# Performance work log

Measured on AMD Instinct MI355X. Metric: run time of the kernel, lower is better.

## Reference

```python
import jax, jax.numpy as jnp
import numpy as np

N_NODES = 50000
N_EDGES = 800000
D_IN = 128
D_OUT = 128
N_TYPES = 4
LN_EPS = 1e-5


def setup_inputs() -> dict:
    key = jax.random.key(0)
    ks = jax.random.split(key, 12)
    s1 = 1.0 / np.sqrt(2 * D_IN)
    s2 = 1.0 / np.sqrt(D_OUT)
    return {
        "x": jax.random.normal(ks[0], (N_NODES, D_IN), jnp.float32),
        "edge_index": jax.random.randint(ks[1], (2, N_EDGES), 0, N_NODES, jnp.int32),
        "edge_attr": jax.random.randint(ks[2], (N_EDGES,), 0, N_TYPES, jnp.int32),
        # per-edge-type 2-layer MLP params, stacked over type axis
        "edge_w1": jax.random.uniform(ks[3], (N_TYPES, 2 * D_IN, D_OUT), jnp.float32, -s1, s1),
        "edge_b1": jax.random.uniform(ks[4], (N_TYPES, D_OUT), jnp.float32, -s1, s1),
        "edge_w2": jax.random.uniform(ks[5], (N_TYPES, D_OUT, D_OUT), jnp.float32, -s2, s2),
        "edge_b2": jax.random.uniform(ks[6], (N_TYPES, D_OUT), jnp.float32, -s2, s2),
        "self_w": jax.random.uniform(ks[7], (D_IN, D_OUT), jnp.float32, -s2, s2),
        "self_b": jax.random.uniform(ks[8], (D_OUT,), jnp.float32, -s2, s2),
        "ln_gamma": jnp.ones((D_OUT,), jnp.float32),
        "ln_beta": jnp.zeros((D_OUT,), jnp.float32),
    }


def reference(x, edge_index, edge_attr, edge_w1, edge_b1, edge_w2, edge_b2, self_w, self_b, ln_gamma, ln_beta):
    row, col = edge_index[0], edge_index[1]
    out = x @ self_w + self_b  # (N, D_OUT) self-loop

    # gather once: (E, 2*D_IN)
    ef = jnp.concatenate([x[row], x[col]], axis=1)

    # per-edge-type MLP; masked edges contribute exactly zero, matching the
    # boolean-mask + index_add_ semantics of the original.
    msg = jnp.zeros((ef.shape[0], edge_w2.shape[-1]), dtype=x.dtype)
    for t in range(edge_w1.shape[0]):
        h = jax.nn.relu(ef @ edge_w1[t] + edge_b1[t])
        m = h @ edge_w2[t] + edge_b2[t]
        msg = msg + jnp.where((edge_attr == t)[:, None], m, 0.0)

    out = out + jax.ops.segment_sum(msg, col, num_segments=x.shape[0])

    # ReLU then LayerNorm over feature dim
    h = jax.nn.relu(out)
    mu = jnp.mean(h, axis=-1, keepdims=True)
    var = jnp.mean(jnp.square(h - mu), axis=-1, keepdims=True)
    return (h - mu) * jax.lax.rsqrt(var + LN_EPS) * ln_gamma + ln_beta
```

## Files before the change

kernel.cpp:

```cpp
#include <hip/hip_runtime.h>

#define N_NODES 50000
#define N_EDGES 800000
#define D_IN 128
#define D_OUT 128
#define N_TYPES 4
#define LN_EPS 1e-5f
#define N_BUCKETS (N_TYPES * N_NODES)
#define NJT 9

#define NBIN 196
#define BIN_CAP 8192
#define TILE_A 2048
#define NBA ((N_EDGES + TILE_A - 1) / TILE_A)

typedef __attribute__((ext_vector_type(4))) float f32x4;
typedef __attribute__((ext_vector_type(8))) __bf16 bf16x8;
typedef __attribute__((ext_vector_type(8))) unsigned short u16x8;

constexpr size_t wsal(size_t x) { return (x + 255) & ~size_t(255); }
constexpr size_t OFF_PTR    = 0;
constexpr size_t OFF_BCUR   = OFF_PTR   + wsal((size_t)(N_BUCKETS + 1) * 4);
constexpr size_t OFF_BINBUF = OFF_BCUR  + wsal((size_t)256 * 4);
constexpr size_t OFF_SROWS  = OFF_BINBUF + wsal((size_t)NBIN * BIN_CAP * 4);
constexpr size_t OFF_XB     = OFF_SROWS + wsal((size_t)N_EDGES * 4);
constexpr size_t OFF_WCAT   = OFF_XB    + wsal((size_t)N_NODES * D_IN * 2);
constexpr size_t OFF_BIAS   = OFF_WCAT  + wsal((size_t)NJT * 4 * 128 * 32 * 2);
constexpr size_t OFF_W2T    = OFF_BIAS  + wsal((size_t)NJT * 128 * 4);
constexpr size_t OFF_XAB    = OFF_W2T   + wsal((size_t)N_TYPES * 4 * 128 * 32 * 2);
constexpr size_t OFF_S      = OFF_XAB   + wsal((size_t)8 * N_NODES * 128 * 2);
constexpr size_t WS_TOTAL   = OFF_S     + wsal((size_t)N_BUCKETS * 128 * 2);

__device__ __forceinline__ unsigned short f2bf(float f) {
    unsigned int u = __builtin_bit_cast(unsigned int, f);
    u += 0x7FFFu + ((u >> 16) & 1u);
    return (unsigned short)(u >> 16);
}
__device__ __forceinline__ float bf2f_lo(unsigned int u) { return __builtin_bit_cast(float, u << 16); }
__device__ __forceinline__ float bf2f_hi(unsigned int u) { return __builtin_bit_cast(float, u & 0xFFFF0000u); }

#define PREP_N0 (NJT * 4 * 128 * 32)
#define PREP_N1 (NJT * 128)
#define PREP_N2 (N_TYPES * 4 * 128 * 32)
#define NB_CVT  (N_NODES * D_IN / 4 / 256)
#define NB_PREP ((PREP_N0 + PREP_N1 + PREP_N2 + 255) / 256)

__global__ __launch_bounds__(256) void k_prep_all(
    const float* __restrict__ x,
    const float* __restrict__ w1, const float* __restrict__ sw,
    const float* __restrict__ b1, const float* __restrict__ sb,
    const float* __restrict__ w2,
    unsigned short* __restrict__ xb,
    unsigned short* __restrict__ wcatT, float* __restrict__ bias,
    unsigned short* __restrict__ w2T)
{
    const int bx = blockIdx.x;
    const int tid = threadIdx.x;
    if (bx < NB_CVT) {
        int i = bx * 256 + tid;
        const float4 v = reinterpret_cast<const float4*>(x)[i];
        ushort4 o;
        o.x = f2bf(v.x); o.y = f2bf(v.y); o.z = f2bf(v.z); o.w = f2bf(v.w);
        reinterpret_cast<ushort4*>(xb)[i] = o;
        return;
    }
    int gid = (bx - NB_CVT) * 256 + tid;
    if (gid < PREP_N0) {
        int kk = gid & 31;
        int jm = (gid >> 5) & 127;
        int ks = (gid >> 12) & 3;
        int jt = gid >> 14;
        int k  = ks * 32 + kk;
        float v;
        if (jt < 8) {
            int t = jt >> 1, half = jt & 1;
            v = w1[((size_t)t * 256 + half * 128 + k) * 128 + jm];
        } else {
            v = sw[(size_t)k * 128 + jm];
        }
        wcatT[gid] = f2bf(v);
        return;
    }
    gid -= PREP_N0;
    if (gid < PREP_N1) {
        int jt = gid >> 7, jm = gid & 127;
        float v = 0.f;
        if (jt < 8) { if (jt & 1) v = b1[(jt >> 1) * 128 + jm]; }
        else v = sb[jm];
        bias[gid] = v;
        return;
    }
    gid -= PREP_N1;
    if (gid < PREP_N2) {
        int kk = gid & 31;
        int f  = (gid >> 5) & 127;
        int ks = (gid >> 12) & 3;
        int t  = gid >> 14;
        float v = w2[((size_t)t * 128 + ks * 32 + kk) * 128 + f];
        w2T[gid] = f2bf(v);
    }
}

__global__ __launch_bounds__(256) void k_binA(
    const int* __restrict__ ei, const int* __restrict__ attr,
    int* __restrict__ binCur, unsigned int* __restrict__ binBuf)
{
    __shared__ int hist[NBIN];
    __shared__ int base[NBIN];
    const int tid = threadIdx.x;
    const int e0 = blockIdx.x * TILE_A;
    if (tid < NBIN) hist[tid] = 0;
    __syncthreads();
    #pragma unroll
    for (int it = 0; it < TILE_A / 256; ++it) {
        int e = e0 + it * 256 + tid;
        if (e < N_EDGES) atomicAdd(&hist[ei[N_EDGES + e] >> 8], 1);
    }
    __syncthreads();
    if (tid < NBIN) {
        base[tid] = atomicAdd(&binCur[tid], hist[tid]);
        hist[tid] = 0;
    }
    __syncthreads();
    #pragma unroll
    for (int it = 0; it < TILE_A / 256; ++it) {
        int e = e0 + it * 256 + tid;
        if (e < N_EDGES) {
            int c = ei[N_EDGES + e];
            int t = attr[e];
            int row = ei[e];
            int bin = c >> 8;
            int lr = atomicAdd(&hist[bin], 1);
            int dst = base[bin] + lr;
            unsigned int rec = ((unsigned int)(c & 255) << 21) | ((unsigned int)t << 19)
                             | (unsigned int)(2 * t * N_NODES + row);
            if (dst < BIN_CAP) binBuf[(size_t)bin * BIN_CAP + dst] = rec;
        }
    }
}

__global__ __launch_bounds__(256) void k_binB(
    const unsigned int* __restrict__ binBuf, const int* __restrict__ binCur,
    int* __restrict__ ptr, int* __restrict__ srows)
{
    __shared__ unsigned int recs[BIN_CAP];
    __shared__ int stage[BIN_CAP];
    __shared__ int boff[1024];
    __shared__ int sred[256];
    const int b = blockIdx.x, tid = threadIdx.x;
    const int cntb = min(binCur[b], BIN_CAP);

    for (int i = tid; i < cntb; i += 256)
        recs[i] = binBuf[(size_t)b * BIN_CAP + i];

    int myv = (tid < NBIN && tid < b) ? binCur[tid] : 0;
    sred[tid] = myv;
    __syncthreads();
    #pragma unroll
    for (int d = 128; d > 0; d >>= 1) {
        if (tid < d) sred[tid] += sred[tid + d];
        __syncthreads();
    }
    const int binBase = sred[0];
    __syncthreads();

    for (int k = tid; k < 1024; k += 256) boff[k] = 0;
    __syncthreads();
    for (int i = tid; i < cntb; i += 256)
        atomicAdd(&boff[(recs[i] >> 19) & 1023], 1);
    __syncthreads();

    const int c0 = boff[tid * 4], c1 = boff[tid * 4 + 1], c2 = boff[tid * 4 + 2], c3 = boff[tid * 4 + 3];
    const int ts = c0 + c1 + c2 + c3;
    sred[tid] = ts;
    __syncthreads();
    #pragma unroll
    for (int d = 1; d < 256; d <<= 1) {
        int add = (tid >= d) ? sred[tid - d] : 0;
        __syncthreads();
        sred[tid] += add;
        __syncthreads();
    }
    const int run = sred[tid] - ts;
    const int o0 = run, o1 = run + c0, o2 = run + c0 + c1, o3 = run + c0 + c1 + c2;
    boff[tid * 4 + 0] = o0; boff[tid * 4 + 1] = o1;
    boff[tid * 4 + 2] = o2; boff[tid * 4 + 3] = o3;
    const int gb = b * 1024 + tid * 4;
    if (gb + 3 < N_BUCKETS) {
        int4 pv; pv.x = binBase + o0; pv.y = binBase + o1; pv.z = binBase + o2; pv.w = binBase + o3;
        *reinterpret_cast<int4*>(ptr + gb) = pv;
    } else {
        if (gb + 0 < N_BUCKETS) ptr[gb + 0] = binBase + o0;
        if (gb + 1 < N_BUCKETS) ptr[gb + 1] = binBase + o1;
        if (gb + 2 < N_BUCKETS) ptr[gb + 2] = binBase + o2;
        if (gb + 3 < N_BUCKETS) ptr[gb + 3] = binBase + o3;
    }
    if (b == 0 && tid == 0) ptr[N_BUCKETS] = N_EDGES;
    __syncthreads();

    for (int i = tid; i < cntb; i += 256) {
        unsigned int r = recs[i];
        int pos = atomicAdd(&boff[(r >> 19) & 1023], 1);
        stage[pos] = (int)(r & 0x7FFFFu);
    }
    __syncthreads();
    for (int i = tid; i < cntb; i += 256)
        srows[binBase + i] = stage[i];
}

__global__ __launch_bounds__(256, 2) void k_gemm1(
    const unsigned short* __restrict__ xb,
    const unsigned short* __restrict__ wcatT,
    const float* __restrict__ bias,
    unsigned short* __restrict__ xab)
{
    const int nb = blockIdx.x * 128;
    const int jt = blockIdx.y;

    __shared__ __align__(16) unsigned short sX[128 * 136];
    __shared__ __align__(16) unsigned short sW[4 * 128 * 32];

    const int tid = threadIdx.x;
    const int lane = tid & 63;
    const int w = tid >> 6;
    const int g = lane >> 4;
    const int c = lane & 15;
    const int wf = w >> 1;
    const int we = w & 1;

    #pragma unroll
    for (int it = 0; it < 8; ++it) {
        int row = 16 * it + (tid >> 4);
        int node = min(nb + row, N_NODES - 1);
        const u16x8 v = *reinterpret_cast<const u16x8*>(xb + (size_t)node * D_IN + (tid & 15) * 8);
        *reinterpret_cast<u16x8*>(&sX[row * 136 + (tid & 15) * 8]) = v;
    }
    {
        const u16x8* gsrc = reinterpret_cast<const u16x8*>(wcatT + (size_t)jt * 16384);
        u16x8* ldst = reinterpret_cast<u16x8*>(sW);
        #pragma unroll
        for (int it = 0; it < 8; ++it)
            ldst[tid + 256 * it] = gsrc[tid + 256 * it];
    }

    f32x4 acc[4][4];
    #pragma unroll
    for (int ft = 0; ft < 4; ++ft)
        #pragma unroll
        for (int et = 0; et < 4; ++et)
            acc[ft][et] = f32x4{0.f, 0.f, 0.f, 0.f};

    __syncthreads();

    #pragma unroll
    for (int ks = 0; ks < 4; ++ks) {
        bf16x8 af[4], bfr[4];
        #pragma unroll
        for (int ft = 0; ft < 4; ++ft)
            af[ft] = *reinterpret_cast<const bf16x8*>(&sW[ks * 4096 + (64 * wf + 16 * ft + c) * 32 + 8 * g]);
        #pragma unroll
        for (int et = 0; et < 4; ++et)
            bfr[et] = *reinterpret_cast<const bf16x8*>(&sX[(64 * we + 16 * et + c) * 136 + ks * 32 + 8 * g]);
        #pragma unroll
        for (int ft = 0; ft < 4; ++ft)
            #pragma unroll
            for (int et = 0; et < 4; ++et)
                acc[ft][et] = __builtin_amdgcn_mfma_f32_16x16x32_bf16(af[ft], bfr[et], acc[ft][et], 0, 0, 0);
    }
    __syncthreads();

    {
        float bv[4][4];
        #pragma unroll
        for (int ft = 0; ft < 4; ++ft)
            #pragma unroll
            for (int r = 0; r < 4; ++r)
                bv[ft][r] = bias[jt * 128 + 64 * wf + 16 * ft + 4 * g + r];
        unsigned int* so = reinterpret_cast<unsigned int*>(sX);
        #pragma unroll
        for (int ft = 0; ft < 4; ++ft) {
            #pragma unroll
            for (int et = 0; et < 4; ++et) {
                int n = 64 * we + 16 * et + c;
                int jb = 32 * wf + 8 * ft + 2 * g;
                float v0 = acc[ft][et][0] + bv[ft][0];
                float v1 = acc[ft][et][1] + bv[ft][1];
                float v2 = acc[ft][et][2] + bv[ft][2];
                float v3 = acc[ft][et][3] + bv[ft][3];
                so[n * 68 + jb + 0] = (unsigned int)f2bf(v0) | ((unsigned int)f2bf(v1) << 16);
                so[n * 68 + jb + 1] = (unsigned int)f2bf(v2) | ((unsigned int)f2bf(v3) << 16);
            }
        }
    }
    __syncthreads();

    #pragma unroll
    for (int it = 0; it < 8; ++it) {
        int row = 16 * it + (tid >> 4);
        int node = nb + row;
        if (node < N_NODES) {
            const u16x8 v = *reinterpret_cast<const u16x8*>(&sX[row * 136 + (tid & 15) * 8]);
            *reinterpret_cast<u16x8*>(xab + ((size_t)jt * N_NODES + node) * 128 + (tid & 15) * 8) = v;
        }
    }
}

__global__ __launch_bounds__(256) void k_agg(const unsigned short* __restrict__ xab,
                                             const int* __restrict__ ptr,
                                             const int* __restrict__ srows,
                                             unsigned short* __restrict__ S)
{
    const int n = (blockIdx.x * 256 + threadIdx.x) >> 6;
    if (n >= N_NODES) return;
    const int lane = threadIdx.x & 63;
    const unsigned int* x32 = reinterpret_cast<const unsigned int*>(xab);

    int seg[5];
    #pragma unroll
    for (int t = 0; t < 5; ++t)
        seg[t] = __builtin_amdgcn_readfirstlane(ptr[4 * n + t]);

    float xbl[4], xbh[4];
    #pragma unroll
    for (int t = 0; t < 4; ++t) {
        unsigned int v = x32[((size_t)(2 * t + 1) * N_NODES + n) * 64 + lane];
        xbl[t] = bf2f_lo(v); xbh[t] = bf2f_hi(v);
    }

    float al[4] = {0.f, 0.f, 0.f, 0.f}, ah[4] = {0.f, 0.f, 0.f, 0.f};

    #pragma unroll
    for (int t = 0; t < 4; ++t) {
        const int lo = seg[t], hi = seg[t + 1];
        int j = lo;
        for (; j + 4 <= hi; j += 4) {
            int a0 = __builtin_amdgcn_readfirstlane(srows[j]);
            int a1 = __builtin_amdgcn_readfirstlane(srows[j + 1]);
            int a2 = __builtin_amdgcn_readfirstlane(srows[j + 2]);
            int a3 = __builtin_amdgcn_readfirstlane(srows[j + 3]);
            unsigned int v0 = x32[(size_t)a0 * 64 + lane];
            unsigned int v1 = x32[(size_t)a1 * 64 + lane];
            unsigned int v2 = x32[(size_t)a2 * 64 + lane];
            unsigned int v3 = x32[(size_t)a3 * 64 + lane];
            al[t] += fmaxf(bf2f_lo(v0) + xbl[t], 0.f) + fmaxf(bf2f_lo(v1) + xbl[t], 0.f)
                   + fmaxf(bf2f_lo(v2) + xbl[t], 0.f) + fmaxf(bf2f_lo(v3) + xbl[t], 0.f);
            ah[t] += fmaxf(bf2f_hi(v0) + xbh[t], 0.f) + fmaxf(bf2f_hi(v1) + xbh[t], 0.f)
                   + fmaxf(bf2f_hi(v2) + xbh[t], 0.f) + fmaxf(bf2f_hi(v3) + xbh[t], 0.f);
        }
        for (; j < hi; ++j) {
            int a = __builtin_amdgcn_readfirstlane(srows[j]);
            unsigned int v = x32[(size_t)a * 64 + lane];
            al[t] += fmaxf(bf2f_lo(v) + xbl[t], 0.f);
            ah[t] += fmaxf(bf2f_hi(v) + xbh[t], 0.f);
        }
    }

    unsigned int* S32 = reinterpret_cast<unsigned int*>(S);
    #pragma unroll
    for (int t = 0; t < 4; ++t)
        S32[((size_t)n * 4 + t) * 64 + lane] =
            (unsigned int)f2bf(al[t]) | ((unsigned int)f2bf(ah[t]) << 16);
}

__global__ __launch_bounds__(256, 2) void k_gemm2_ln(
    const unsigned short* __restrict__ S,
    const unsigned short* __restrict__ w2T,
    const unsigned short* __restrict__ wcatT,
    const unsigned short* __restrict__ xb,
    const float* __restrict__ b2,
    const float* __restrict__ sb,
    const int* __restrict__ ptr,
    const float* __restrict__ gamma,
    const float* __restrict__ beta,
    float* __restrict__ out)
{
    const int nb = blockIdx.x * 128;
    __shared__ __align__(16) unsigned char sm[128 * 136 * 2 + 4 * 128 * 32 * 2 + 512 * 4];
    unsigned short* sS  = reinterpret_cast<unsigned short*>(sm);
    unsigned short* sW2 = reinterpret_cast<unsigned short*>(sm + 34816);
    float* sB2          = reinterpret_cast<float*>(sm + 34816 + 32768);
    float* rows         = reinterpret_cast<float*>(sm);

    const int tid = threadIdx.x;
    const int lane = tid & 63;
    const int w = tid >> 6;
    const int g = lane >> 4;
    const int c = lane & 15;
    const int wf = w >> 1;
    const int we = w & 1;

    sB2[tid] = b2[tid];
    sB2[tid + 256] = b2[tid + 256];

    f32x4 acc[4][4];
    #pragma unroll
    for (int ft = 0; ft < 4; ++ft)
        #pragma unroll
        for (int et = 0; et < 4; ++et)
            acc[ft][et] = f32x4{0.f, 0.f, 0.f, 0.f};

    for (int t = 0; t < 5; ++t) {
        const unsigned short* srcW = (t < 4) ? w2T + (size_t)t * 16384 : wcatT + (size_t)8 * 16384;
        __syncthreads();
        #pragma unroll
        for (int it = 0; it < 8; ++it) {
            int row = 16 * it + (tid >> 4);
            int node = min(nb + row, N_NODES - 1);
            const unsigned short* src = (t < 4)
                ? S + ((size_t)node * 4 + t) * 128
                : xb + (size_t)node * 128;
            const u16x8 v = *reinterpret_cast<const u16x8*>(src + (tid & 15) * 8);
            *reinterpret_cast<u16x8*>(&sS[row * 136 + (tid & 15) * 8]) = v;
        }
        {
            const u16x8* gsrc = reinterpret_cast<const u16x8*>(srcW);
            u16x8* ldst = reinterpret_cast<u16x8*>(sW2);
            #pragma unroll
            for (int it = 0; it < 8; ++it)
                ldst[tid + 256 * it] = gsrc[tid + 256 * it];
        }
        __syncthreads();
        #pragma unroll
        for (int ks = 0; ks < 4; ++ks) {
            bf16x8 af[4], bfr[4];
            #pragma unroll
            for (int ft = 0; ft < 4; ++ft)
                af[ft] = *reinterpret_cast<const bf16x8*>(&sW2[ks * 4096 + (64 * wf + 16 * ft + c) * 32 + 8 * g]);
            #pragma unroll
            for (int et = 0; et < 4; ++et)
                bfr[et] = *reinterpret_cast<const bf16x8*>(&sS[(64 * we + 16 * et + c) * 136 + ks * 32 + 8 * g]);
            #pragma unroll
            for (int ft = 0; ft < 4; ++ft)
                #pragma unroll
                for (int et = 0; et < 4; ++et)
                    acc[ft][et] = __builtin_amdgcn_mfma_f32_16x16x32_bf16(af[ft], bfr[et], acc[ft][et], 0, 0, 0);
        }
    }
    __syncthreads();

    #pragma unroll
    for (int et = 0; et < 4; ++et) {
        int n = 64 * we + 16 * et + c;
        int node = nb + n;
        if (node >= N_NODES) continue;
        const int4 pv4 = *reinterpret_cast<const int4*>(ptr + node * 4);
        const int pe = ptr[node * 4 + 4];
        float cnt4[N_TYPES] = {(float)(pv4.y - pv4.x), (float)(pv4.z - pv4.y),
                               (float)(pv4.w - pv4.z), (float)(pe - pv4.w)};
        #pragma unroll
        for (int ft = 0; ft < 4; ++ft) {
            int f0 = 64 * wf + 16 * ft + 4 * g;
            const float4 sbv = *reinterpret_cast<const float4*>(sb + f0);
            float v[4];
            v[0] = acc[ft][et][0] + sbv.x;
            v[1] = acc[ft][et][1] + sbv.y;
            v[2] = acc[ft][et][2] + sbv.z;
            v[3] = acc[ft][et][3] + sbv.w;
            #pragma unroll
            for (int r = 0; r < 4; ++r) {
                float bs = 0.f;
                #pragma unroll
                for (int t = 0; t < N_TYPES; ++t)
                    bs = fmaf(cnt4[t], sB2[t * 128 + f0 + r], bs);
                v[r] += bs;
            }
            *reinterpret_cast<float4*>(&rows[n * 132 + f0]) = *reinterpret_cast<float4*>(v);
        }
    }
    __syncthreads();

    for (int rr = 0; rr < 32; ++rr) {
        int r = w * 32 + rr;
        int node = nb + r;
        if (node >= N_NODES) break;
        float2 v = *reinterpret_cast<float2*>(&rows[r * 132 + lane * 2]);
        v.x = fmaxf(v.x, 0.f);
        v.y = fmaxf(v.y, 0.f);
        float s = v.x + v.y;
        float ss = v.x * v.x + v.y * v.y;
        #pragma unroll
        for (int m = 1; m < 64; m <<= 1) {
            s  += __shfl_xor(s, m, 64);
            ss += __shfl_xor(ss, m, 64);
        }
        float mu = s * (1.f / 128.f);
        float var = ss * (1.f / 128.f) - mu * mu;
        float rs = rsqrtf(var + LN_EPS);
        const float2 gm = *reinterpret_cast<const float2*>(gamma + lane * 2);
        const float2 bt = *reinterpret_cast<const float2*>(beta + lane * 2);
        float2 o;
        o.x = (v.x - mu) * rs * gm.x + bt.x;
        o.y = (v.y - mu) * rs * gm.y + bt.y;
        *reinterpret_cast<float2*>(out + (size_t)node * D_OUT + lane * 2) = o;
    }
}

extern "C" void kernel_launch(void* const* d_in, const int* in_sizes, int n_in,
                              void* d_out, int out_size, void* d_ws, size_t ws_size,
                              hipStream_t stream) {
    const float* x     = (const float*)d_in[0];
    const int*   ei    = (const int*)d_in[1];
    const int*   attr  = (const int*)d_in[2];
    const float* w1    = (const float*)d_in[3];
    const float* b1    = (const float*)d_in[4];
    const float* w2    = (const float*)d_in[5];
    const float* b2    = (const float*)d_in[6];
    const float* sw    = (const float*)d_in[7];
    const float* sb    = (const float*)d_in[8];
    const float* gamma = (const float*)d_in[9];
    const float* beta  = (const float*)d_in[10];
    float* out = (float*)d_out;

    if (ws_size < WS_TOTAL) return;

    char* ws = (char*)d_ws;
    int* ptr    = (int*)(ws + OFF_PTR);
    int* binCur = (int*)(ws + OFF_BCUR);
    unsigned int* binBuf = (unsigned int*)(ws + OFF_BINBUF);
    int* srows  = (int*)(ws + OFF_SROWS);
    unsigned short* xb    = (unsigned short*)(ws + OFF_XB);
    unsigned short* wcatT = (unsigned short*)(ws + OFF_WCAT);
    float*          bias  = (float*)(ws + OFF_BIAS);
    unsigned short* w2T   = (unsigned short*)(ws + OFF_W2T);
    unsigned short* xab   = (unsigned short*)(ws + OFF_XAB);
    unsigned short* S     = (unsigned short*)(ws + OFF_S);

    hipMemsetAsync(binCur, 0, (size_t)NBIN * 4, stream);

    k_prep_all<<<NB_CVT + NB_PREP, 256, 0, stream>>>(
        x, w1, sw, b1, sb, w2, xb, wcatT, bias, w2T);

    k_binA<<<NBA, 256, 0, stream>>>(ei, attr, binCur, binBuf);
    k_binB<<<NBIN, 256, 0, stream>>>(binBuf, binCur, ptr, srows);

    k_gemm1<<<dim3((N_NODES + 127) / 128, 8), 256, 0, stream>>>(xb, wcatT, bias, xab);
    k_agg<<<(N_NODES * 64 + 255) / 256, 256, 0, stream>>>(xab, ptr, srows, S);
    k_gemm2_ln<<<(N_NODES + 127) / 128, 256, 0, stream>>>(
        S, w2T, wcatT, xb, b2, sb, ptr, gamma, beta, out);
}
```

Measured before the change: 160.7 us.

## Drop weight LDS staging, shrink LDS footprint, batch edge-index loads per wave

Both GEMM kernels now read weight fragments straight from global memory (L2-resident) instead of staging them in shared memory. The epilogue of gemm2 stores the pre-LayerNorm rows as bf16 in the reused sS buffer instead of a larger fp32 staging area. Together these cut LDS use per block, so launch bounds rise to 4 blocks per CU to raise occupancy. The aggregation kernel loads 64 edge source indices per wave in one vector load and broadcasts them with readlane, replacing per-edge scalar loads. The risks are more global/L2 traffic for weights, register pressure under the tighter launch bound, and some precision loss from rounding LN inputs to bf16.

```diff
diff --git a/kernel.cpp b/kernel.cpp
--- a/kernel.cpp
+++ b/kernel.cpp
@@ -208,7 +208,7 @@
         srows[binBase + i] = stage[i];
 }
 
-__global__ __launch_bounds__(256, 2) void k_gemm1(
+__global__ __launch_bounds__(256, 4) void k_gemm1(
     const unsigned short* __restrict__ xb,
     const unsigned short* __restrict__ wcatT,
     const float* __restrict__ bias,
@@ -218,7 +218,6 @@
     const int jt = blockIdx.y;
 
     __shared__ __align__(16) unsigned short sX[128 * 136];
-    __shared__ __align__(16) unsigned short sW[4 * 128 * 32];
 
     const int tid = threadIdx.x;
     const int lane = tid & 63;
@@ -235,13 +234,6 @@
         const u16x8 v = *reinterpret_cast<const u16x8*>(xb + (size_t)node * D_IN + (tid & 15) * 8);
         *reinterpret_cast<u16x8*>(&sX[row * 136 + (tid & 15) * 8]) = v;
     }
-    {
-        const u16x8* gsrc = reinterpret_cast<const u16x8*>(wcatT + (size_t)jt * 16384);
-        u16x8* ldst = reinterpret_cast<u16x8*>(sW);
-        #pragma unroll
-        for (int it = 0; it < 8; ++it)
-            ldst[tid + 256 * it] = gsrc[tid + 256 * it];
-    }
 
     f32x4 acc[4][4];
     #pragma unroll
@@ -252,12 +244,13 @@
 
     __syncthreads();
 
+    const unsigned short* wbase = wcatT + (size_t)jt * 16384;
     #pragma unroll
     for (int ks = 0; ks < 4; ++ks) {
         bf16x8 af[4], bfr[4];
         #pragma unroll
         for (int ft = 0; ft < 4; ++ft)
-            af[ft] = *reinterpret_cast<const bf16x8*>(&sW[ks * 4096 + (64 * wf + 16 * ft + c) * 32 + 8 * g]);
+            af[ft] = *reinterpret_cast<const bf16x8*>(wbase + ks * 4096 + (64 * wf + 16 * ft + c) * 32 + 8 * g);
         #pragma unroll
         for (int et = 0; et < 4; ++et)
             bfr[et] = *reinterpret_cast<const bf16x8*>(&sX[(64 * we + 16 * et + c) * 136 + ks * 32 + 8 * g]);
@@ -329,29 +322,36 @@
 
     float al[4] = {0.f, 0.f, 0.f, 0.f}, ah[4] = {0.f, 0.f, 0.f, 0.f};
 
-    #pragma unroll
-    for (int t = 0; t < 4; ++t) {
-        const int lo = seg[t], hi = seg[t + 1];
-        int j = lo;
-        for (; j + 4 <= hi; j += 4) {
-            int a0 = __builtin_amdgcn_readfirstlane(srows[j]);
-            int a1 = __builtin_amdgcn_readfirstlane(srows[j + 1]);
-            int a2 = __builtin_amdgcn_readfirstlane(srows[j + 2]);
-            int a3 = __builtin_amdgcn_readfirstlane(srows[j + 3]);
-            unsigned int v0 = x32[(size_t)a0 * 64 + lane];
-            unsigned int v1 = x32[(size_t)a1 * 64 + lane];
-            unsigned int v2 = x32[(size_t)a2 * 64 + lane];
-            unsigned int v3 = x32[(size_t)a3 * 64 + lane];
-            al[t] += fmaxf(bf2f_lo(v0) + xbl[t], 0.f) + fmaxf(bf2f_lo(v1) + xbl[t], 0.f)
-                   + fmaxf(bf2f_lo(v2) + xbl[t], 0.f) + fmaxf(bf2f_lo(v3) + xbl[t], 0.f);
-            ah[t] += fmaxf(bf2f_hi(v0) + xbh[t], 0.f) + fmaxf(bf2f_hi(v1) + xbh[t], 0.f)
-                   + fmaxf(bf2f_hi(v2) + xbh[t], 0.f) + fmaxf(bf2f_hi(v3) + xbh[t], 0.f);
-        }
-        for (; j < hi; ++j) {
-            int a = __builtin_amdgcn_readfirstlane(srows[j]);
-            unsigned int v = x32[(size_t)a * 64 + lane];
-            al[t] += fmaxf(bf2f_lo(v) + xbl[t], 0.f);
-            ah[t] += fmaxf(bf2f_hi(v) + xbh[t], 0.f);
+    const int p0 = seg[0], pE = seg[4];
+    for (int co = p0; co < pE; co += 64) {
+        const int rem = pE - co;
+        const int cv = srows[co + min(lane, rem - 1)];
+        const int ce = min(co + 64, pE);
+        #pragma unroll
+        for (int t = 0; t < 4; ++t) {
+            const int lo = max(seg[t], co);
+            const int hi = min(seg[t + 1], ce);
+            int j = lo;
+            for (; j + 4 <= hi; j += 4) {
+                int a0 = __builtin_amdgcn_readlane(cv, j - co);
+                int a1 = __builtin_amdgcn_readlane(cv, j + 1 - co);
+                int a2 = __builtin_amdgcn_readlane(cv, j + 2 - co);
+                int a3 = __builtin_amdgcn_readlane(cv, j + 3 - co);
+                unsigned int v0 = x32[(size_t)a0 * 64 + lane];
+                unsigned int v1 = x32[(size_t)a1 * 64 + lane];
+                unsigned int v2 = x32[(size_t)a2 * 64 + lane];
+                unsigned int v3 = x32[(size_t)a3 * 64 + lane];
+                al[t] += fmaxf(bf2f_lo(v0) + xbl[t], 0.f) + fmaxf(bf2f_lo(v1) + xbl[t], 0.f)
+                       + fmaxf(bf2f_lo(v2) + xbl[t], 0.f) + fmaxf(bf2f_lo(v3) + xbl[t], 0.f);
+                ah[t] += fmaxf(bf2f_hi(v0) + xbh[t], 0.f) + fmaxf(bf2f_hi(v1) + xbh[t], 0.f)
+                       + fmaxf(bf2f_hi(v2) + xbh[t], 0.f) + fmaxf(bf2f_hi(v3) + xbh[t], 0.f);
+            }
+            for (; j < hi; ++j) {
+                int a = __builtin_amdgcn_readlane(cv, j - co);
+                unsigned int v = x32[(size_t)a * 64 + lane];
+                al[t] += fmaxf(bf2f_lo(v) + xbl[t], 0.f);
+                ah[t] += fmaxf(bf2f_hi(v) + xbh[t], 0.f);
+            }
         }
     }
 
@@ -362,7 +362,7 @@
             (unsigned int)f2bf(al[t]) | ((unsigned int)f2bf(ah[t]) << 16);
 }
 
-__global__ __launch_bounds__(256, 2) void k_gemm2_ln(
+__global__ __launch_bounds__(256, 4) void k_gemm2_ln(
     const unsigned short* __restrict__ S,
     const unsigned short* __restrict__ w2T,
     const unsigned short* __restrict__ wcatT,
@@ -375,11 +375,8 @@
     float* __restrict__ out)
 {
     const int nb = blockIdx.x * 128;
-    __shared__ __align__(16) unsigned char sm[128 * 136 * 2 + 4 * 128 * 32 * 2 + 512 * 4];
-    unsigned short* sS  = reinterpret_cast<unsigned short*>(sm);
-    unsigned short* sW2 = reinterpret_cast<unsigned short*>(sm + 34816);
-    float* sB2          = reinterpret_cast<float*>(sm + 34816 + 32768);
-    float* rows         = reinterpret_cast<float*>(sm);
+    __shared__ __align__(16) unsigned short sS[128 * 136];
+    __shared__ float sB2[512];
 
     const int tid = threadIdx.x;
     const int lane = tid & 63;
@@ -400,7 +397,6 @@
             acc[ft][et] = f32x4{0.f, 0.f, 0.f, 0.f};
 
     for (int t = 0; t < 5; ++t) {
-        const unsigned short* srcW = (t < 4) ? w2T + (size_t)t * 16384 : wcatT + (size_t)8 * 16384;
         __syncthreads();
         #pragma unroll
         for (int it = 0; it < 8; ++it) {
@@ -412,20 +408,14 @@
             const u16x8 v = *reinterpret_cast<const u16x8*>(src + (tid & 15) * 8);
             *reinterpret_cast<u16x8*>(&sS[row * 136 + (tid & 15) * 8]) = v;
         }
-        {
-            const u16x8* gsrc = reinterpret_cast<const u16x8*>(srcW);
-            u16x8* ldst = reinterpret_cast<u16x8*>(sW2);
-            #pragma unroll
-            for (int it = 0; it < 8; ++it)
-                ldst[tid + 256 * it] = gsrc[tid + 256 * it];
-        }
         __syncthreads();
+        const unsigned short* wbase = (t < 4) ? w2T + (size_t)t * 16384 : wcatT + (size_t)8 * 16384;
         #pragma unroll
         for (int ks = 0; ks < 4; ++ks) {
             bf16x8 af[4], bfr[4];
             #pragma unroll
             for (int ft = 0; ft < 4; ++ft)
-                af[ft] = *reinterpret_cast<const bf16x8*>(&sW2[ks * 4096 + (64 * wf + 16 * ft + c) * 32 + 8 * g]);
+                af[ft] = *reinterpret_cast<const bf16x8*>(wbase + ks * 4096 + (64 * wf + 16 * ft + c) * 32 + 8 * g);
             #pragma unroll
             for (int et = 0; et < 4; ++et)
                 bfr[et] = *reinterpret_cast<const bf16x8*>(&sS[(64 * we + 16 * et + c) * 136 + ks * 32 + 8 * g]);
@@ -438,44 +428,50 @@
     }
     __syncthreads();
 
-    #pragma unroll
-    for (int et = 0; et < 4; ++et) {
-        int n = 64 * we + 16 * et + c;
-        int node = nb + n;
-        if (node >= N_NODES) continue;
-        const int4 pv4 = *reinterpret_cast<const int4*>(ptr + node * 4);
-        const int pe = ptr[node * 4 + 4];
-        float cnt4[N_TYPES] = {(float)(pv4.y - pv4.x), (float)(pv4.z - pv4.y),
-                               (float)(pv4.w - pv4.z), (float)(pe - pv4.w)};
-        #pragma unroll
-        for (int ft = 0; ft < 4; ++ft) {
-            int f0 = 64 * wf + 16 * ft + 4 * g;
-            const float4 sbv = *reinterpret_cast<const float4*>(sb + f0);
-            float v[4];
-            v[0] = acc[ft][et][0] + sbv.x;
-            v[1] = acc[ft][et][1] + sbv.y;
-            v[2] = acc[ft][et][2] + sbv.z;
-            v[3] = acc[ft][et][3] + sbv.w;
-            #pragma unroll
-            for (int r = 0; r < 4; ++r) {
-                float bs = 0.f;
+    {
+        unsigned int* so = reinterpret_cast<unsigned int*>(sS);
+        #pragma unroll
+        for (int et = 0; et < 4; ++et) {
+            int n = 64 * we + 16 * et + c;
+            int node = nb + n;
+            if (node >= N_NODES) continue;
+            const int4 pv4 = *reinterpret_cast<const int4*>(ptr + node * 4);
+            const int pe = ptr[node * 4 + 4];
+            float cnt4[N_TYPES] = {(float)(pv4.y - pv4.x), (float)(pv4.z - pv4.y),
+                                   (float)(pv4.w - pv4.z), (float)(pe - pv4.w)};
+            #pragma unroll
+            for (int ft = 0; ft < 4; ++ft) {
+                int f0 = 64 * wf + 16 * ft + 4 * g;
+                const float4 sbv = *reinterpret_cast<const float4*>(sb + f0);
+                float v[4];
+                v[0] = acc[ft][et][0] + sbv.x;
+                v[1] = acc[ft][et][1] + sbv.y;
+                v[2] = acc[ft][et][2] + sbv.z;
+                v[3] = acc[ft][et][3] + sbv.w;
                 #pragma unroll
-                for (int t = 0; t < N_TYPES; ++t)
-                    bs = fmaf(cnt4[t], sB2[t * 128 + f0 + r], bs);
-                v[r] += bs;
+                for (int r = 0; r < 4; ++r) {
+                    float bs = 0.f;
+                    #pragma unroll
+                    for (int t = 0; t < N_TYPES; ++t)
+                        bs = fmaf(cnt4[t], sB2[t * 128 + f0 + r], bs);
+                    v[r] = fmaxf(v[r] + bs, 0.f);
+                }
+                so[n * 68 + (f0 >> 1) + 0] = (unsigned int)f2bf(v[0]) | ((unsigned int)f2bf(v[1]) << 16);
+                so[n * 68 + (f0 >> 1) + 1] = (unsigned int)f2bf(v[2]) | ((unsigned int)f2bf(v[3]) << 16);
             }
-            *reinterpret_cast<float4*>(&rows[n * 132 + f0]) = *reinterpret_cast<float4*>(v);
-        }
-    }
-    __syncthreads();
-
+        }
+    }
+    __syncthreads();
+
+    const unsigned int* so = reinterpret_cast<const unsigned int*>(sS);
     for (int rr = 0; rr < 32; ++rr) {
         int r = w * 32 + rr;
         int node = nb + r;
         if (node >= N_NODES) break;
-        float2 v = *reinterpret_cast<float2*>(&rows[r * 132 + lane * 2]);
-        v.x = fmaxf(v.x, 0.f);
-        v.y = fmaxf(v.y, 0.f);
+        unsigned int pv = so[r * 68 + lane];
+        float2 v;
+        v.x = bf2f_lo(pv);
+        v.y = bf2f_hi(pv);
         float s = v.x + v.y;
         float ss = v.x * v.x + v.y * v.y;
         #pragma unroll
```

Result: slower. 205.1 us (+27.6%).

## Loop weight tiles inside gemm1 and load edge indices per wave in agg

Applied to the files above, without the earlier changes.

k_gemm1 now launches one block per 128-node tile and loops over all 8 weight column tiles. The X tile is loaded once into LDS and reused for every tile. Outputs are written straight from registers to global memory instead of being staged through LDS. In k_agg, each wave loads 64 source indices at once with a coalesced load and reads them with readlane, replacing the scalar load per edge. The trade-off is fewer blocks in gemm1 (391 instead of 3128), which lowers parallelism, and scattered 8-byte global stores.

```diff
diff --git a/kernel.cpp b/kernel.cpp
--- a/kernel.cpp
+++ b/kernel.cpp
@@ -215,10 +215,9 @@
     unsigned short* __restrict__ xab)
 {
     const int nb = blockIdx.x * 128;
-    const int jt = blockIdx.y;
 
     __shared__ __align__(16) unsigned short sX[128 * 136];
-    __shared__ __align__(16) unsigned short sW[4 * 128 * 32];
+    __shared__ __align__(16) unsigned short sW[128 * 136];
 
     const int tid = threadIdx.x;
     const int lane = tid & 63;
@@ -235,73 +234,71 @@
         const u16x8 v = *reinterpret_cast<const u16x8*>(xb + (size_t)node * D_IN + (tid & 15) * 8);
         *reinterpret_cast<u16x8*>(&sX[row * 136 + (tid & 15) * 8]) = v;
     }
-    {
-        const u16x8* gsrc = reinterpret_cast<const u16x8*>(wcatT + (size_t)jt * 16384);
-        u16x8* ldst = reinterpret_cast<u16x8*>(sW);
-        #pragma unroll
-        for (int it = 0; it < 8; ++it)
-            ldst[tid + 256 * it] = gsrc[tid + 256 * it];
-    }
-
-    f32x4 acc[4][4];
-    #pragma unroll
-    for (int ft = 0; ft < 4; ++ft)
-        #pragma unroll
-        for (int et = 0; et < 4; ++et)
-            acc[ft][et] = f32x4{0.f, 0.f, 0.f, 0.f};
-
-    __syncthreads();
-
-    #pragma unroll
-    for (int ks = 0; ks < 4; ++ks) {
-        bf16x8 af[4], bfr[4];
+
+    for (int jt = 0; jt < 8; ++jt) {
+        {
+            const u16x8* gsrc = reinterpret_cast<const u16x8*>(wcatT + (size_t)jt * 16384);
+            #pragma unroll
+            for (int it = 0; it < 8; ++it) {
+                int idx = it * 256 + tid;
+                int ks = idx >> 9;
+                int f  = (idx >> 2) & 127;
+                int k8 = idx & 3;
+                const u16x8 v = gsrc[idx];
+                *reinterpret_cast<u16x8*>(&sW[f * 136 + ks * 32 + k8 * 8]) = v;
+            }
+        }
+        __syncthreads();
+
+        f32x4 acc[4][4];
         #pragma unroll
         for (int ft = 0; ft < 4; ++ft)
-            af[ft] = *reinterpret_cast<const bf16x8*>(&sW[ks * 4096 + (64 * wf + 16 * ft + c) * 32 + 8 * g]);
-        #pragma unroll
-        for (int et = 0; et < 4; ++et)
-            bfr[et] = *reinterpret_cast<const bf16x8*>(&sX[(64 * we + 16 * et + c) * 136 + ks * 32 + 8 * g]);
-        #pragma unroll
-        for (int ft = 0; ft < 4; ++ft)
             #pragma unroll
             for (int et = 0; et < 4; ++et)
-                acc[ft][et] = __builtin_amdgcn_mfma_f32_16x16x32_bf16(af[ft], bfr[et], acc[ft][et], 0, 0, 0);
-    }
-    __syncthreads();
-
-    {
+                acc[ft][et] = f32x4{0.f, 0.f, 0.f, 0.f};
+
+        #pragma unroll
+        for (int ks = 0; ks < 4; ++ks) {
+            bf16x8 af[4], bfr[4];
+            #pragma unroll
+            for (int ft = 0; ft < 4; ++ft)
+                af[ft] = *reinterpret_cast<const bf16x8*>(&sW[(64 * wf + 16 * ft + c) * 136 + ks * 32 + 8 * g]);
+            #pragma unroll
+            for (int et = 0; et < 4; ++et)
+                bfr[et] = *reinterpret_cast<const bf16x8*>(&sX[(64 * we + 16 * et + c) * 136 + ks * 32 + 8 * g]);
+            #pragma unroll
+            for (int ft = 0; ft < 4; ++ft)
+                #pragma unroll
+                for (int et = 0; et < 4; ++et)
+                    acc[ft][et] = __builtin_amdgcn_mfma_f32_16x16x32_bf16(af[ft], bfr[et], acc[ft][et], 0, 0, 0);
+        }
+
         float bv[4][4];
         #pragma unroll
         for (int ft = 0; ft < 4; ++ft)
             #pragma unroll
             for (int r = 0; r < 4; ++r)
                 bv[ft][r] = bias[jt * 128 + 64 * wf + 16 * ft + 4 * g + r];
-        unsigned int* so = reinterpret_cast<unsigned int*>(sX);
-        #pragma unroll
-        for (int ft = 0; ft < 4; ++ft) {
-            #pragma unroll
-            for (int et = 0; et < 4; ++et) {
-                int n = 64 * we + 16 * et + c;
-                int jb = 32 * wf + 8 * ft + 2 * g;
-                float v0 = acc[ft][et][0] + bv[ft][0];
-                float v1 = acc[ft][et][1] + bv[ft][1];
-                float v2 = acc[ft][et][2] + bv[ft][2];
-                float v3 = acc[ft][et][3] + bv[ft][3];
-                so[n * 68 + jb + 0] = (unsigned int)f2bf(v0) | ((unsigned int)f2bf(v1) << 16);
-                so[n * 68 + jb + 1] = (unsigned int)f2bf(v2) | ((unsigned int)f2bf(v3) << 16);
+        #pragma unroll
+        for (int et = 0; et < 4; ++et) {
+            int n = 64 * we + 16 * et + c;
+            int node = nb + n;
+            if (node < N_NODES) {
+                unsigned int* orow = reinterpret_cast<unsigned int*>(
+                    xab + ((size_t)jt * N_NODES + node) * 128);
+                #pragma unroll
+                for (int ft = 0; ft < 4; ++ft) {
+                    int f0 = 64 * wf + 16 * ft + 4 * g;
+                    uint2 pk;
+                    pk.x = (unsigned int)f2bf(acc[ft][et][0] + bv[ft][0])
+                         | ((unsigned int)f2bf(acc[ft][et][1] + bv[ft][1]) << 16);
+                    pk.y = (unsigned int)f2bf(acc[ft][et][2] + bv[ft][2])
+                         | ((unsigned int)f2bf(acc[ft][et][3] + bv[ft][3]) << 16);
+                    *reinterpret_cast<uint2*>(orow + (f0 >> 1)) = pk;
+                }
             }
         }
-    }
-    __syncthreads();
-
-    #pragma unroll
-    for (int it = 0; it < 8; ++it) {
-        int row = 16 * it + (tid >> 4);
-        int node = nb + row;
-        if (node < N_NODES) {
-            const u16x8 v = *reinterpret_cast<const u16x8*>(&sX[row * 136 + (tid & 15) * 8]);
-            *reinterpret_cast<u16x8*>(xab + ((size_t)jt * N_NODES + node) * 128 + (tid & 15) * 8) = v;
-        }
+        __syncthreads();
     }
 }
 
@@ -329,29 +326,36 @@
 
     float al[4] = {0.f, 0.f, 0.f, 0.f}, ah[4] = {0.f, 0.f, 0.f, 0.f};
 
-    #pragma unroll
-    for (int t = 0; t < 4; ++t) {
-        const int lo = seg[t], hi = seg[t + 1];
-        int j = lo;
-        for (; j + 4 <= hi; j += 4) {
-            int a0 = __builtin_amdgcn_readfirstlane(srows[j]);
-            int a1 = __builtin_amdgcn_readfirstlane(srows[j + 1]);
-            int a2 = __builtin_amdgcn_readfirstlane(srows[j + 2]);
-            int a3 = __builtin_amdgcn_readfirstlane(srows[j + 3]);
-            unsigned int v0 = x32[(size_t)a0 * 64 + lane];
-            unsigned int v1 = x32[(size_t)a1 * 64 + lane];
-            unsigned int v2 = x32[(size_t)a2 * 64 + lane];
-            unsigned int v3 = x32[(size_t)a3 * 64 + lane];
-            al[t] += fmaxf(bf2f_lo(v0) + xbl[t], 0.f) + fmaxf(bf2f_lo(v1) + xbl[t], 0.f)
-                   + fmaxf(bf2f_lo(v2) + xbl[t], 0.f) + fmaxf(bf2f_lo(v3) + xbl[t], 0.f);
-            ah[t] += fmaxf(bf2f_hi(v0) + xbh[t], 0.f) + fmaxf(bf2f_hi(v1) + xbh[t], 0.f)
-                   + fmaxf(bf2f_hi(v2) + xbh[t], 0.f) + fmaxf(bf2f_hi(v3) + xbh[t], 0.f);
-        }
-        for (; j < hi; ++j) {
-            int a = __builtin_amdgcn_readfirstlane(srows[j]);
-            unsigned int v = x32[(size_t)a * 64 + lane];
-            al[t] += fmaxf(bf2f_lo(v) + xbl[t], 0.f);
-            ah[t] += fmaxf(bf2f_hi(v) + xbh[t], 0.f);
+    const int p0 = seg[0], pE = seg[4];
+    for (int co = p0; co < pE; co += 64) {
+        const int rem = pE - co;
+        const int cv = srows[co + min(lane, rem - 1)];
+        const int ce = min(co + 64, pE);
+        #pragma unroll
+        for (int t = 0; t < 4; ++t) {
+            const int lo = max(seg[t], co);
+            const int hi = min(seg[t + 1], ce);
+            int j = lo;
+            for (; j + 4 <= hi; j += 4) {
+                int a0 = __builtin_amdgcn_readlane(cv, j - co);
+                int a1 = __builtin_amdgcn_readlane(cv, j + 1 - co);
+                int a2 = __builtin_amdgcn_readlane(cv, j + 2 - co);
+                int a3 = __builtin_amdgcn_readlane(cv, j + 3 - co);
+                unsigned int v0 = x32[(size_t)a0 * 64 + lane];
+                unsigned int v1 = x32[(size_t)a1 * 64 + lane];
+                unsigned int v2 = x32[(size_t)a2 * 64 + lane];
+                unsigned int v3 = x32[(size_t)a3 * 64 + lane];
+                al[t] += fmaxf(bf2f_lo(v0) + xbl[t], 0.f) + fmaxf(bf2f_lo(v1) + xbl[t], 0.f)
+                       + fmaxf(bf2f_lo(v2) + xbl[t], 0.f) + fmaxf(bf2f_lo(v3) + xbl[t], 0.f);
+                ah[t] += fmaxf(bf2f_hi(v0) + xbh[t], 0.f) + fmaxf(bf2f_hi(v1) + xbh[t], 0.f)
+                       + fmaxf(bf2f_hi(v2) + xbh[t], 0.f) + fmaxf(bf2f_hi(v3) + xbh[t], 0.f);
+            }
+            for (; j < hi; ++j) {
+                int a = __builtin_amdgcn_readlane(cv, j - co);
+                unsigned int v = x32[(size_t)a * 64 + lane];
+                al[t] += fmaxf(bf2f_lo(v) + xbl[t], 0.f);
+                ah[t] += fmaxf(bf2f_hi(v) + xbh[t], 0.f);
+            }
         }
     }
 
@@ -533,7 +537,7 @@
     k_binA<<<NBA, 256, 0, stream>>>(ei, attr, binCur, binBuf);
     k_binB<<<NBIN, 256, 0, stream>>>(binBuf, binCur, ptr, srows);
 
-    k_gemm1<<<dim3((N_NODES + 127) / 128, 8), 256, 0, stream>>>(xb, wcatT, bias, xab);
+    k_gemm1<<<(N_NODES + 127) / 128, 256, 0, stream>>>(xb, wcatT, bias, xab);
     k_agg<<<(N_NODES * 64 + 255) / 256, 256, 0, stream>>>(xab, ptr, srows, S);
     k_gemm2_ln<<<(N_NODES + 127) / 128, 256, 0, stream>>>(
         S, w2T, wcatT, xb, b2, sb, ptr, gamma, beta, out);
```

Result: slower. 167.8 us (+4.4%).
